# Optimization experiments

Measured on AMD Instinct MI355X. Metric: run time of the kernel, lower is better.

The kernel has to match this reference:

```python
import jax, jax.numpy as jnp
import numpy as np

N_NODES = 100000
N_EDGES = 1600000
D_FEAT = 64


def setup_inputs() -> dict:
    key = jax.random.key(0)
    k1, k2, k3 = jax.random.split(key, 3)
    h = jax.random.normal(k1, (N_NODES, D_FEAT), dtype=jnp.float32)
    src = jax.random.randint(k2, (N_EDGES,), 0, N_NODES, dtype=jnp.int32)
    dst = jax.random.randint(k3, (N_EDGES,), 0, N_NODES, dtype=jnp.int32)
    edge_index = jnp.stack([src, dst], axis=0)  # [2, E]
    return {"h": h, "edge_index": edge_index}


def reference(h, edge_index):
    # EdgePassing: message = src node features (gather along edges)
    # Max_aggregation: per-dst-node max over incoming messages (segment max)
    src, dst = edge_index[0], edge_index[1]
    msgs = h[src]  # [E, D] gathered mailbox, never densified per-node
    agg = jax.ops.segment_max(msgs, dst, num_segments=N_NODES)  # [N, D]
    # DGL leaves nodes with no incoming messages at zero; segment_max yields -inf
    return jnp.where(jnp.isneginf(agg), jnp.zeros_like(agg), agg)
```

## Files before the change

### kernel.cpp

```cpp
#include <hip/hip_runtime.h>
#include <stdint.h>

#define D_FEAT 64
#define NEG_INF_BITS 0xFF800000u
#define ENC_NEG_INF  0x007FFFFFu
#define NPB 64
#define BSHIFT 6
#define BM_BLOCK 512
#define MAXB 2048

__device__ __forceinline__ unsigned enc_f32(float v) {
    unsigned b = __float_as_uint(v);
    return ((int)b >= 0) ? (b ^ 0x80000000u) : ~b;
}
__device__ __forceinline__ float dec_f32(unsigned u) {
    return (u & 0x80000000u) ? __uint_as_float(u ^ 0x80000000u) : __uint_as_float(~u);
}

__global__ void count_kernel(const int* __restrict__ dst, int* __restrict__ hist,
                             int E, int B, int aligned4) {
    __shared__ int lh[MAXB];
    for (int i = threadIdx.x; i < B; i += blockDim.x) lh[i] = 0;
    __syncthreads();
    int gid = blockIdx.x * blockDim.x + threadIdx.x;
    int gstride = gridDim.x * blockDim.x;
    int n4 = aligned4 ? (E >> 2) : 0;
    const int4* d4 = (const int4*)dst;
    for (int k = gid; k < n4; k += gstride) {
        int4 d = d4[k];
        atomicAdd(&lh[d.x >> BSHIFT], 1);
        atomicAdd(&lh[d.y >> BSHIFT], 1);
        atomicAdd(&lh[d.z >> BSHIFT], 1);
        atomicAdd(&lh[d.w >> BSHIFT], 1);
    }
    for (int i = (n4 << 2) + gid; i < E; i += gstride)
        atomicAdd(&lh[dst[i] >> BSHIFT], 1);
    __syncthreads();
    for (int i = threadIdx.x; i < B; i += blockDim.x) {
        int c = lh[i];
        if (c) atomicAdd(&hist[i], c);
    }
}

__global__ void scan_kernel(const int* __restrict__ hist, int* __restrict__ bucket_start,
                            int* __restrict__ cursor, int B) {
    __shared__ int lds[MAXB / 2];
    int tid = threadIdx.x;
    int i0 = 2 * tid, i1 = 2 * tid + 1;
    int v0 = (i0 < B) ? hist[i0] : 0;
    int v1 = (i1 < B) ? hist[i1] : 0;
    int s = v0 + v1;
    lds[tid] = s;
    __syncthreads();
    for (int off = 1; off < (MAXB / 2); off <<= 1) {
        int t = (tid >= off) ? lds[tid - off] : 0;
        __syncthreads();
        lds[tid] += t;
        __syncthreads();
    }
    int excl = lds[tid] - s;
    if (i0 < B) { bucket_start[i0] = excl;      cursor[i0] = excl; }
    if (i1 < B) { bucket_start[i1] = excl + v0; cursor[i1] = excl + v0; }
    if (tid == (MAXB / 2) - 1) bucket_start[B] = lds[tid];
}

__global__ void place_kernel(const int* __restrict__ src, const int* __restrict__ dst,
                             int* __restrict__ cursor, unsigned* __restrict__ packed,
                             int E, int Te, int B, int aligned4) {
    __shared__ int lh[MAXB];
    int t = blockIdx.x;
    int beg = t * Te;
    int end = min(E, beg + Te);
    if (beg >= end) return;
    for (int i = threadIdx.x; i < B; i += blockDim.x) lh[i] = 0;
    __syncthreads();
    int nE = end - beg;
    int n4 = aligned4 ? (nE >> 2) : 0;
    const int4* d4 = (const int4*)(dst + beg);
    for (int k = threadIdx.x; k < n4; k += blockDim.x) {
        int4 d = d4[k];
        atomicAdd(&lh[d.x >> BSHIFT], 1);
        atomicAdd(&lh[d.y >> BSHIFT], 1);
        atomicAdd(&lh[d.z >> BSHIFT], 1);
        atomicAdd(&lh[d.w >> BSHIFT], 1);
    }
    for (int i = beg + (n4 << 2) + threadIdx.x; i < end; i += blockDim.x)
        atomicAdd(&lh[dst[i] >> BSHIFT], 1);
    __syncthreads();
    for (int i = threadIdx.x; i < B; i += blockDim.x) {
        int c = lh[i];
        lh[i] = c ? atomicAdd(&cursor[i], c) : 0;
    }
    __syncthreads();
    for (int i = beg + threadIdx.x; i < end; i += blockDim.x) {
        int d = dst[i];
        int b = d >> BSHIFT;
        int pos = atomicAdd(&lh[b], 1);
        packed[pos] = (unsigned)src[i] | ((unsigned)(d & (NPB - 1)) << 17);
    }
}

__global__ void __launch_bounds__(BM_BLOCK)
bucket_max_kernel(const float* __restrict__ h,
                  const int* __restrict__ bucket_start,
                  const unsigned* __restrict__ packed,
                  float* __restrict__ out, int N) {
    __shared__ unsigned buf[NPB * D_FEAT];
    int b = blockIdx.x;
    int tid = threadIdx.x;
    int node0 = b << BSHIFT;
    int nvals = (min(NPB, N - node0)) * D_FEAT;

    for (int i = tid; i < NPB * D_FEAT; i += BM_BLOCK) buf[i] = ENC_NEG_INF;
    __syncthreads();

    int beg = bucket_start[b];
    int end = bucket_start[b + 1];
    int wid = tid >> 6;
    int lane = tid & 63;

    for (int base = beg + (wid << 6); base < end; base += BM_BLOCK) {
        int nk = min(64, end - base);
        unsigned p = (lane < nk) ? packed[base + lane] : 0u;
        int j = 0;
        for (; j + 8 <= nk; j += 8) {
            unsigned q[8];
            float v[8];
            #pragma unroll
            for (int k = 0; k < 8; ++k) q[k] = (unsigned)__shfl((int)p, j + k);
            #pragma unroll
            for (int k = 0; k < 8; ++k) v[k] = h[(q[k] & 0x1FFFFu) * D_FEAT + lane];
            #pragma unroll
            for (int k = 0; k < 8; ++k)
                atomicMax(&buf[(q[k] >> 17) * D_FEAT + lane], enc_f32(v[k]));
        }
        for (; j < nk; ++j) {
            unsigned pj = (unsigned)__shfl((int)p, j);
            float v = h[(pj & 0x1FFFFu) * D_FEAT + lane];
            atomicMax(&buf[(pj >> 17) * D_FEAT + lane], enc_f32(v));
        }
    }
    __syncthreads();

    for (int i = tid; i < nvals; i += BM_BLOCK) {
        unsigned u = buf[i];
        out[node0 * D_FEAT + i] = (u == ENC_NEG_INF) ? 0.0f : dec_f32(u);
    }
}

__global__ void init_out_kernel(uint4* __restrict__ out, int n4) {
    int i = blockIdx.x * blockDim.x + threadIdx.x;
    if (i < n4) {
        uint4 v;
        v.x = NEG_INF_BITS; v.y = NEG_INF_BITS; v.z = NEG_INF_BITS; v.w = NEG_INF_BITS;
        out[i] = v;
    }
}
__global__ void scatter_max_kernel(const float* __restrict__ h, const int* __restrict__ src,
                                   const int* __restrict__ dst, float* __restrict__ out, int E) {
    int gid = blockIdx.x * blockDim.x + threadIdx.x;
    int e = gid >> 6;
    if (e >= E) return;
    int lane = gid & 63;
    float v = h[src[e] * D_FEAT + lane];
    int* addr = (int*)(out + dst[e] * D_FEAT + lane);
    if (v >= 0.0f) atomicMax(addr, __float_as_int(v));
    else           atomicMin((unsigned int*)addr, __float_as_uint(v));
}
__global__ void finalize_kernel(float* __restrict__ out, int n) {
    int i = blockIdx.x * blockDim.x + threadIdx.x;
    if (i < n && __float_as_uint(out[i]) == NEG_INF_BITS) out[i] = 0.0f;
}

extern "C" void kernel_launch(void* const* d_in, const int* in_sizes, int n_in,
                              void* d_out, int out_size, void* d_ws, size_t ws_size,
                              hipStream_t stream) {
    const float* h = (const float*)d_in[0];
    const int* edge_index = (const int*)d_in[1];
    int E = in_sizes[1] / 2;
    const int* src = edge_index;
    const int* dst = edge_index + E;
    float* out = (float*)d_out;
    int N = out_size / D_FEAT;

    int B = (N + NPB - 1) >> BSHIFT;
    size_t need = ((size_t)3 * B + 1 + (size_t)E) * sizeof(int);

    if (N <= (1 << 17) && B <= MAXB && E > 0 && ws_size >= need) {
        int* hist         = (int*)d_ws;
        int* bucket_start = hist + B;
        int* cursor       = bucket_start + B + 1;
        unsigned* packed  = (unsigned*)(cursor + B);

        int aligned4 = ((((uintptr_t)dst) & 15) == 0) ? 1 : 0;

        hipMemsetAsync(hist, 0, (size_t)B * sizeof(int), stream);

        count_kernel<<<256, 512, 0, stream>>>(dst, hist, E, B, aligned4);
        scan_kernel<<<1, MAXB / 2, 0, stream>>>(hist, bucket_start, cursor, B);
        int Te = ((E + 255) / 256 + 3) & ~3;
        int pblocks = (E + Te - 1) / Te;
        place_kernel<<<pblocks, 512, 0, stream>>>(src, dst, cursor, packed, E, Te, B, aligned4);
        bucket_max_kernel<<<B, BM_BLOCK, 0, stream>>>(h, bucket_start, packed, out, N);
    } else {
        int n4 = out_size / 4;
        init_out_kernel<<<(n4 + 255) / 256, 256, 0, stream>>>((uint4*)out, n4);
        long long total = (long long)E * 64;
        scatter_max_kernel<<<(int)((total + 255) / 256), 256, 0, stream>>>(h, src, dst, out, E);
        finalize_kernel<<<(out_size + 255) / 256, 256, 0, stream>>>(out, out_size);
    }
}
```

Before: 176.6 us.

## Vectorize placement loop, retune place/hist/bucket-max launch shapes, vectorize output writes

The placement pass now reads src and dst as int4 and scatters four packed entries per iteration. It uses 64 blocks of 1024 threads instead of 256 blocks of 512. The histogram grid doubles to 512 blocks, and the bucket-max block shrinks to 256 threads. The bucket-max epilogue decodes results with integer bit operations and writes uint4 stores for full buckets. Together these aim to cut load instruction count and launch overhead, at the cost of fewer placement blocks and less parallelism per bucket.

Measured after the change: 182.2 us. 3.2% more time.

```diff
diff --git a/kernel.cpp b/kernel.cpp
--- a/kernel.cpp
+++ b/kernel.cpp
@@ -6,19 +6,22 @@
 #define ENC_NEG_INF  0x007FFFFFu
 #define NPB 64
 #define BSHIFT 6
-#define BM_BLOCK 512
+#define BM_BLOCK 256
 #define MAXB 2048
+#define PL_BLOCKS 64
+#define PL_THREADS 1024
 
 __device__ __forceinline__ unsigned enc_f32(float v) {
     unsigned b = __float_as_uint(v);
     return ((int)b >= 0) ? (b ^ 0x80000000u) : ~b;
 }
-__device__ __forceinline__ float dec_f32(unsigned u) {
-    return (u & 0x80000000u) ? __uint_as_float(u ^ 0x80000000u) : __uint_as_float(~u);
-}
-
-__global__ void count_kernel(const int* __restrict__ dst, int* __restrict__ hist,
-                             int E, int B, int aligned4) {
+__device__ __forceinline__ unsigned dec_bits(unsigned u) {
+    if (u == ENC_NEG_INF) return 0u;
+    return (u & 0x80000000u) ? (u ^ 0x80000000u) : ~u;
+}
+
+__global__ void hist_kernel(const int* __restrict__ dst, int* __restrict__ hist,
+                            int E, int B, int aligned4) {
     __shared__ int lh[MAXB];
     for (int i = threadIdx.x; i < B; i += blockDim.x) lh[i] = 0;
     __syncthreads();
@@ -64,9 +67,10 @@
     if (tid == (MAXB / 2) - 1) bucket_start[B] = lds[tid];
 }
 
-__global__ void place_kernel(const int* __restrict__ src, const int* __restrict__ dst,
-                             int* __restrict__ cursor, unsigned* __restrict__ packed,
-                             int E, int Te, int B, int aligned4) {
+__global__ void __launch_bounds__(PL_THREADS)
+place_kernel(const int* __restrict__ src, const int* __restrict__ dst,
+             int* __restrict__ cursor, unsigned* __restrict__ packed,
+             int E, int Te, int B, int aligned4) {
     __shared__ int lh[MAXB];
     int t = blockIdx.x;
     int beg = t * Te;
@@ -77,6 +81,7 @@
     int nE = end - beg;
     int n4 = aligned4 ? (nE >> 2) : 0;
     const int4* d4 = (const int4*)(dst + beg);
+    const int4* s4 = (const int4*)(src + beg);
     for (int k = threadIdx.x; k < n4; k += blockDim.x) {
         int4 d = d4[k];
         atomicAdd(&lh[d.x >> BSHIFT], 1);
@@ -92,10 +97,21 @@
         lh[i] = c ? atomicAdd(&cursor[i], c) : 0;
     }
     __syncthreads();
-    for (int i = beg + threadIdx.x; i < end; i += blockDim.x) {
+    for (int k = threadIdx.x; k < n4; k += blockDim.x) {
+        int4 d = d4[k];
+        int4 s = s4[k];
+        int p0 = atomicAdd(&lh[d.x >> BSHIFT], 1);
+        packed[p0] = (unsigned)s.x | ((unsigned)(d.x & (NPB - 1)) << 17);
+        int p1 = atomicAdd(&lh[d.y >> BSHIFT], 1);
+        packed[p1] = (unsigned)s.y | ((unsigned)(d.y & (NPB - 1)) << 17);
+        int p2 = atomicAdd(&lh[d.z >> BSHIFT], 1);
+        packed[p2] = (unsigned)s.z | ((unsigned)(d.z & (NPB - 1)) << 17);
+        int p3 = atomicAdd(&lh[d.w >> BSHIFT], 1);
+        packed[p3] = (unsigned)s.w | ((unsigned)(d.w & (NPB - 1)) << 17);
+    }
+    for (int i = beg + (n4 << 2) + threadIdx.x; i < end; i += blockDim.x) {
         int d = dst[i];
-        int b = d >> BSHIFT;
-        int pos = atomicAdd(&lh[b], 1);
+        int pos = atomicAdd(&lh[d >> BSHIFT], 1);
         packed[pos] = (unsigned)src[i] | ((unsigned)(d & (NPB - 1)) << 17);
     }
 }
@@ -129,22 +145,32 @@
             #pragma unroll
             for (int k = 0; k < 8; ++k) q[k] = (unsigned)__shfl((int)p, j + k);
             #pragma unroll
-            for (int k = 0; k < 8; ++k) v[k] = h[(q[k] & 0x1FFFFu) * D_FEAT + lane];
+            for (int k = 0; k < 8; ++k) v[k] = h[(size_t)(q[k] & 0x1FFFFu) * D_FEAT + lane];
             #pragma unroll
             for (int k = 0; k < 8; ++k)
                 atomicMax(&buf[(q[k] >> 17) * D_FEAT + lane], enc_f32(v[k]));
         }
         for (; j < nk; ++j) {
             unsigned pj = (unsigned)__shfl((int)p, j);
-            float v = h[(pj & 0x1FFFFu) * D_FEAT + lane];
+            float v = h[(size_t)(pj & 0x1FFFFu) * D_FEAT + lane];
             atomicMax(&buf[(pj >> 17) * D_FEAT + lane], enc_f32(v));
         }
     }
     __syncthreads();
 
-    for (int i = tid; i < nvals; i += BM_BLOCK) {
-        unsigned u = buf[i];
-        out[node0 * D_FEAT + i] = (u == ENC_NEG_INF) ? 0.0f : dec_f32(u);
+    if (nvals == NPB * D_FEAT) {
+        uint4* o4 = (uint4*)(out + (size_t)node0 * D_FEAT);
+        const uint4* b4 = (const uint4*)buf;
+        for (int i = tid; i < (NPB * D_FEAT) / 4; i += BM_BLOCK) {
+            uint4 u = b4[i];
+            uint4 r;
+            r.x = dec_bits(u.x); r.y = dec_bits(u.y);
+            r.z = dec_bits(u.z); r.w = dec_bits(u.w);
+            o4[i] = r;
+        }
+    } else {
+        unsigned* o = (unsigned*)(out + (size_t)node0 * D_FEAT);
+        for (int i = tid; i < nvals; i += BM_BLOCK) o[i] = dec_bits(buf[i]);
     }
 }
 
@@ -192,15 +218,13 @@
         int* cursor       = bucket_start + B + 1;
         unsigned* packed  = (unsigned*)(cursor + B);
 
-        int aligned4 = ((((uintptr_t)dst) & 15) == 0) ? 1 : 0;
+        int aligned4 = (((((uintptr_t)dst) | ((uintptr_t)src)) & 15) == 0) ? 1 : 0;
 
         hipMemsetAsync(hist, 0, (size_t)B * sizeof(int), stream);
-
-        count_kernel<<<256, 512, 0, stream>>>(dst, hist, E, B, aligned4);
+        hist_kernel<<<512, 512, 0, stream>>>(dst, hist, E, B, aligned4);
         scan_kernel<<<1, MAXB / 2, 0, stream>>>(hist, bucket_start, cursor, B);
-        int Te = ((E + 255) / 256 + 3) & ~3;
-        int pblocks = (E + Te - 1) / Te;
-        place_kernel<<<pblocks, 512, 0, stream>>>(src, dst, cursor, packed, E, Te, B, aligned4);
+        int Te = ((E + PL_BLOCKS - 1) / PL_BLOCKS + 3) & ~3;
+        place_kernel<<<PL_BLOCKS, PL_THREADS, 0, stream>>>(src, dst, cursor, packed, E, Te, B, aligned4);
         bucket_max_kernel<<<B, BM_BLOCK, 0, stream>>>(h, bucket_start, packed, out, N);
     } else {
         int n4 = out_size / 4;
```
